# Optimization experiments

Measured on AMD Instinct MI355X. Metric: run time of the kernel, lower is better.

The kernel has to match this reference:

```python
import jax, jax.numpy as jnp
import numpy as np

B, S, DIM, H, DH = 1, 4096, 2048, 16, 128
EPS = 1e-5


def setup_inputs() -> dict:
    key = jax.random.key(0)
    ks = jax.random.split(key, 16)
    sc = 0.02
    inp = {
        'hidden_states': jax.random.normal(ks[0], (B, S, DIM), jnp.float32),
        'freqs_cos': jax.random.uniform(ks[1], (1, S, 1, DH), jnp.float32),
        'freqs_sin': jax.random.uniform(ks[2], (1, S, 1, DH), jnp.float32),
        'Wq': jax.random.normal(ks[3], (DIM, DIM), jnp.float32) * sc,
        'bq': jax.random.normal(ks[4], (DIM,), jnp.float32) * sc,
        'Wk': jax.random.normal(ks[5], (DIM, DIM), jnp.float32) * sc,
        'bk': jax.random.normal(ks[6], (DIM,), jnp.float32) * sc,
        'Wv': jax.random.normal(ks[7], (DIM, DIM), jnp.float32) * sc,
        'bv': jax.random.normal(ks[8], (DIM,), jnp.float32) * sc,
        'Wo': jax.random.normal(ks[9], (DIM, DIM), jnp.float32) * sc,
        'bo': jax.random.normal(ks[10], (DIM,), jnp.float32) * sc,
        'gq': jnp.ones((DIM,), jnp.float32),
        'gk': jnp.ones((DIM,), jnp.float32),
    }
    return inp


def _rmsnorm(x, g):
    var = jnp.mean(jnp.square(x), axis=-1, keepdims=True)
    return x * jax.lax.rsqrt(var + EPS) * g


def _apply_rope(x, freqs_cos, freqs_sin):
    # x: [B,S,H,DH]; interleaved rotary as in WanAttnProcessor
    x1 = x[..., 0::2]
    x2 = x[..., 1::2]
    cos = freqs_cos[..., 0::2]
    sin = freqs_sin[..., 1::2]
    o1 = x1 * cos - x2 * sin
    o2 = x1 * sin + x2 * cos
    return jnp.stack([o1, o2], axis=-1).reshape(x.shape)


def reference(hidden_states, freqs_cos, freqs_sin, Wq, bq, Wk, bk, Wv, bv, Wo, bo, gq, gk):
    q = hidden_states @ Wq + bq
    k = hidden_states @ Wk + bk
    v = hidden_states @ Wv + bv
    q = _rmsnorm(q, gq)
    k = _rmsnorm(k, gk)
    q = q.reshape(B, S, H, DH)
    k = k.reshape(B, S, H, DH)
    v = v.reshape(B, S, H, DH)
    q = _apply_rope(q, freqs_cos, freqs_sin)
    k = _apply_rope(k, freqs_cos, freqs_sin)
    scale = 1.0 / np.sqrt(DH).astype(np.float32)
    scores = jnp.einsum('bqhd,bkhd->bhqk', q, k) * scale
    attn = jax.nn.softmax(scores, axis=-1)
    out = jnp.einsum('bhqk,bkhd->bqhd', attn, v)
    out = out.reshape(B, S, H * DH)
    return out @ Wo + bo
```

## Files before the change

kernel.cpp:

```cpp
#include <hip/hip_runtime.h>
#include <hip/hip_bf16.h>

#define SEQ 4096
#define DIMC 2048
#define NH 16
#define DHD 128

typedef short s8v __attribute__((ext_vector_type(8)));
typedef float f4v __attribute__((ext_vector_type(4)));
typedef __bf16 bf8 __attribute__((ext_vector_type(8)));
typedef float f4 __attribute__((ext_vector_type(4)));

typedef __attribute__((address_space(3))) void lds_t;
typedef __attribute__((address_space(1))) void gbl_t;

__device__ __attribute__((aligned(256))) short g_h[(size_t)SEQ * DIMC];
__device__ __attribute__((aligned(256))) short g_q[(size_t)SEQ * DIMC];
__device__ __attribute__((aligned(256))) short g_k[(size_t)SEQ * DIMC];
__device__ __attribute__((aligned(256))) short g_v[(size_t)SEQ * DIMC];
__device__ __attribute__((aligned(256))) short g_vt[(size_t)DIMC * SEQ];
__device__ __attribute__((aligned(256))) short g_wt[4][(size_t)DIMC * DIMC];

__device__ __forceinline__ float b2f(short s) {
    union { unsigned u; float f; } v;
    v.u = ((unsigned)(unsigned short)s) << 16;
    return v.f;
}
__device__ __forceinline__ short f2b(float f) {
    union { float f; unsigned u; } v;
    v.f = f;
    unsigned b = v.u;
    b += 0x7FFFu + ((b >> 16) & 1u);
    return (short)(b >> 16);
}
__device__ __forceinline__ f4 mfma16(bf8 a, bf8 b, f4 c) {
    return __builtin_amdgcn_mfma_f32_16x16x32_bf16(a, b, c, 0, 0, 0);
}
__device__ __forceinline__ void gl_lds16(const short* g, short* l) {
    __builtin_amdgcn_global_load_lds((gbl_t*)g, (lds_t*)l, 16, 0, 0);
}

__global__ __launch_bounds__(256) void conv_h(const float* __restrict__ src) {
    size_t i = ((size_t)blockIdx.x * 256 + threadIdx.x) * 8;
    f4v u0 = *reinterpret_cast<const f4v*>(src + i);
    f4v u1 = *reinterpret_cast<const f4v*>(src + i + 4);
    s8v t;
    for (int j = 0; j < 4; ++j) { t[j] = f2b(u0[j]); t[4 + j] = f2b(u1[j]); }
    *reinterpret_cast<s8v*>(g_h + i) = t;
}

__global__ __launch_bounds__(256) void prep_w(const float* __restrict__ W0,
                                              const float* __restrict__ W1,
                                              const float* __restrict__ W2,
                                              const float* __restrict__ W3) {
    __shared__ __attribute__((aligned(16))) float t[64][68];
    const int z = blockIdx.z;
    const float* W = (z == 0) ? W0 : (z == 1) ? W1 : (z == 2) ? W2 : W3;
    short* WT = g_wt[z];
    const int r0 = blockIdx.y * 64, c0 = blockIdx.x * 64;
    const int tid = threadIdx.x;
    for (int i = 0; i < 4; ++i) {
        int slot = tid + i * 256;
        int r = slot >> 4, c4 = (slot & 15) * 4;
        *reinterpret_cast<f4v*>(&t[r][c4]) =
            *reinterpret_cast<const f4v*>(&W[(size_t)(r0 + r) * DIMC + c0 + c4]);
    }
    __syncthreads();
    for (int i = 0; i < 2; ++i) {
        int slot = tid + i * 256;
        int n = slot >> 3, k8 = (slot & 7) * 8;
        s8v o;
        for (int j = 0; j < 8; ++j) o[j] = f2b(t[k8 + j][n]);
        *reinterpret_cast<s8v*>(&WT[(size_t)(c0 + n) * DIMC + r0 + k8]) = o;
    }
}

template <int DSTF>
__device__ __forceinline__ void gemm_body(const short* __restrict__ X,
                                          const short* __restrict__ Bw,
                                          const float* __restrict__ bias,
                                          short* __restrict__ Yb,
                                          float* __restrict__ Yf,
                                          int bm, int bn) {
    __shared__ __attribute__((aligned(16))) short As[128 * 32];
    __shared__ __attribute__((aligned(16))) short Bs[128 * 32];
    const int tid = threadIdx.x;
    const int w = tid >> 6, lane = tid & 63;
    const int l16 = lane & 15, quad = lane >> 4;
    const int wm = w & 1, wn = w >> 1;

    f4 acc[4][4];
    for (int mi = 0; mi < 4; ++mi)
        for (int ni = 0; ni < 4; ++ni) acc[mi][ni] = (f4)0.0f;

    const int s0 = tid, s1 = tid + 256;
    const int ra0 = s0 >> 2, ca0 = (s0 & 3) * 8;
    const int ra1 = s1 >> 2, ca1 = (s1 & 3) * 8;
    const size_t xo0 = (size_t)(bm * 128 + ra0) * DIMC + ca0;
    const size_t xo1 = (size_t)(bm * 128 + ra1) * DIMC + ca1;
    const size_t bo0 = (size_t)(bn * 128 + ra0) * DIMC + ca0;
    const size_t bo1 = (size_t)(bn * 128 + ra1) * DIMC + ca1;
    short* lda0 = As + (size_t)(0 * 256 + w * 64) * 8;
    short* lda1 = As + (size_t)(1 * 256 + w * 64) * 8;
    short* ldb0 = Bs + (size_t)(0 * 256 + w * 64) * 8;
    short* ldb1 = Bs + (size_t)(1 * 256 + w * 64) * 8;

    for (int kb = 0; kb < DIMC; kb += 32) {
        __syncthreads();
        gl_lds16(X + xo0 + kb, lda0);
        gl_lds16(X + xo1 + kb, lda1);
        gl_lds16(Bw + bo0 + kb, ldb0);
        gl_lds16(Bw + bo1 + kb, ldb1);
        __syncthreads();
        bf8 af[4], bfr[4];
        for (int mi = 0; mi < 4; ++mi)
            af[mi] = *reinterpret_cast<const bf8*>(As + (wm * 64 + mi * 16 + l16) * 32 + quad * 8);
        for (int ni = 0; ni < 4; ++ni)
            bfr[ni] = *reinterpret_cast<const bf8*>(Bs + (wn * 64 + ni * 16 + l16) * 32 + quad * 8);
        for (int mi = 0; mi < 4; ++mi)
            for (int ni = 0; ni < 4; ++ni)
                acc[mi][ni] = mfma16(af[mi], bfr[ni], acc[mi][ni]);
    }

    for (int ni = 0; ni < 4; ++ni) {
        int col = bn * 128 + wn * 64 + ni * 16 + l16;
        float bcol = bias[col];
        for (int mi = 0; mi < 4; ++mi) {
            int row = bm * 128 + wm * 64 + mi * 16 + quad * 4;
            for (int r = 0; r < 4; ++r) {
                if (DSTF)
                    Yf[(size_t)(row + r) * DIMC + col] = acc[mi][ni][r] + bcol;
                else
                    Yb[(size_t)(row + r) * DIMC + col] = f2b(acc[mi][ni][r] + bcol);
            }
        }
    }
}

__global__ __launch_bounds__(256, 2) void gemm_qkv(const float* __restrict__ bq,
                                                   const float* __restrict__ bk,
                                                   const float* __restrict__ bv) {
    const int z = blockIdx.z;
    const float* bias = (z == 0) ? bq : (z == 1) ? bk : bv;
    short* Y = (z == 0) ? g_q : (z == 1) ? g_k : g_v;
    gemm_body<0>(g_h, g_wt[z], bias, Y, nullptr, blockIdx.y, blockIdx.x);
}

__global__ __launch_bounds__(256, 2) void gemm_o(const float* __restrict__ bias,
                                                 float* __restrict__ Yf) {
    gemm_body<1>(g_q, g_wt[3], bias, nullptr, Yf, blockIdx.y, blockIdx.x);
}

__global__ __launch_bounds__(256) void rmsnorm_rope(const float* __restrict__ gq,
                                                    const float* __restrict__ gk,
                                                    const float* __restrict__ fc,
                                                    const float* __restrict__ fs) {
    __shared__ float partial[4];
    __shared__ float totsh;
    const int s = blockIdx.x;
    const int which = blockIdx.y;
    short* x = which ? g_k : g_q;
    const float* g = which ? gk : gq;
    const int tid = threadIdx.x;
    const int d0 = tid * 8;

    s8v xv = *reinterpret_cast<const s8v*>(&x[(size_t)s * DIMC + d0]);
    float xf[8];
    float ssq = 0.0f;
    for (int j = 0; j < 8; ++j) { xf[j] = b2f(xv[j]); ssq += xf[j] * xf[j]; }
    for (int off = 32; off; off >>= 1) ssq += __shfl_down(ssq, off);
    if ((tid & 63) == 0) partial[tid >> 6] = ssq;
    __syncthreads();
    if (tid == 0) totsh = partial[0] + partial[1] + partial[2] + partial[3];
    __syncthreads();
    float rs = rsqrtf(totsh * (1.0f / (float)DIMC) + 1e-5f);
    if (which == 0) rs *= 0.12751744f;

    f4v g0 = *reinterpret_cast<const f4v*>(&g[d0]);
    f4v g1 = *reinterpret_cast<const f4v*>(&g[d0 + 4]);
    float xn[8];
    for (int j = 0; j < 4; ++j) { xn[j] = xf[j] * rs * g0[j]; xn[4 + j] = xf[4 + j] * rs * g1[j]; }

    s8v ov;
    for (int p = 0; p < 4; ++p) {
        int e = d0 + 2 * p;
        int hd = e & (DHD - 1);
        float c = fc[(size_t)s * DHD + hd];
        float sn = fs[(size_t)s * DHD + hd + 1];
        float x1 = xn[2 * p], x2 = xn[2 * p + 1];
        ov[2 * p]     = f2b(x1 * c - x2 * sn);
        ov[2 * p + 1] = f2b(x1 * sn + x2 * c);
    }
    *reinterpret_cast<s8v*>(&x[(size_t)s * DIMC + d0]) = ov;
}

__global__ __launch_bounds__(256) void transpose_v() {
    __shared__ __attribute__((aligned(16))) short t[64][72];
    const int h = blockIdx.z, dt = blockIdx.y, st = blockIdx.x;
    const int tid = threadIdx.x;
    const short* src = g_v + (size_t)st * 64 * DIMC + h * DHD + dt * 64;
    for (int i = 0; i < 2; ++i) {
        int slot = tid + i * 256;
        int s = slot >> 3, d8 = (slot & 7) * 8;
        *reinterpret_cast<s8v*>(&t[s][d8]) =
            *reinterpret_cast<const s8v*>(src + (size_t)s * DIMC + d8);
    }
    __syncthreads();
    short* dst = g_vt + (size_t)(h * DHD + dt * 64) * SEQ + st * 64;
    for (int i = 0; i < 2; ++i) {
        int slot = tid + i * 256;
        int d = slot >> 3, s8_ = (slot & 7) * 8;
        s8v o;
        for (int j = 0; j < 8; ++j) o[j] = t[s8_ + j][d];
        *reinterpret_cast<s8v*>(dst + (size_t)d * SEQ + s8_) = o;
    }
}

__global__ __launch_bounds__(256, 2) void attn_k() {
    __shared__ __attribute__((aligned(16))) short Ks0[2][64 * 128];
    __shared__ __attribute__((aligned(16))) short Vt0[2][128 * 64];
    __shared__ __attribute__((aligned(16))) __hip_bfloat16 Psb[4][16][72];

    const int h = blockIdx.y;
    const int q0 = blockIdx.x * 128;
    const int tid = threadIdx.x;
    const int w = tid >> 6, lane = tid & 63;
    const int l16 = lane & 15, quad = lane >> 4;

    bf8 qf[2][4];
    for (int qs = 0; qs < 2; ++qs) {
        const short* qb = g_q + (size_t)(q0 + w * 32 + qs * 16 + l16) * DIMC + h * DHD + quad * 8;
        for (int c = 0; c < 4; ++c)
            qf[qs][c] = *reinterpret_cast<const bf8*>(qb + c * 32);
    }
    f4 of[2][8];
    for (int qs = 0; qs < 2; ++qs)
        for (int n = 0; n < 8; ++n) of[qs][n] = (f4)0.0f;
    f4 lacc[2] = {(f4)0.0f, (f4)0.0f};

    s8v ob;
    for (int j = 0; j < 8; ++j) ob[j] = (short)0x3F80;
    const bf8 vones = __builtin_bit_cast(bf8, ob);

    const short* Kbase = g_k + h * DHD;
    const short* Vbase = g_vt + (size_t)h * DHD * SEQ;

    const short* kp[4];
    const short* vp[4];
    for (int i = 0; i < 4; ++i) {
        int s = tid + i * 256;
        int krow = s >> 4, kcb = ((s & 15) - krow) & 15;
        int vd = s >> 3, vkb = ((s & 7) - vd) & 7;
        kp[i] = Kbase + (size_t)krow * DIMC + kcb * 8;
        vp[i] = Vbase + (size_t)vd * SEQ + vkb * 8;
    }

    for (int i = 0; i < 4; ++i) {
        gl_lds16(kp[i], &Ks0[0][(size_t)(i * 256 + w * 64) * 8]);
        kp[i] += (size_t)64 * DIMC;
    }
    for (int i = 0; i < 4; ++i) {
        gl_lds16(vp[i], &Vt0[0][(size_t)(i * 256 + w * 64) * 8]);
        vp[i] += 64;
    }

    for (int kt = 0; kt < SEQ; kt += 64) {
        const int cur = (kt >> 6) & 1;
        if (kt + 64 < SEQ) {
            const int nxt = cur ^ 1;
            for (int i = 0; i < 4; ++i) {
                gl_lds16(kp[i], &Ks0[nxt][(size_t)(i * 256 + w * 64) * 8]);
                kp[i] += (size_t)64 * DIMC;
            }
            for (int i = 0; i < 4; ++i) {
                gl_lds16(vp[i], &Vt0[nxt][(size_t)(i * 256 + w * 64) * 8]);
                vp[i] += 64;
            }
            asm volatile("s_waitcnt vmcnt(8)" ::: "memory");
        } else {
            asm volatile("s_waitcnt vmcnt(0)" ::: "memory");
        }
        __builtin_amdgcn_sched_barrier(0);
        __builtin_amdgcn_s_barrier();
        __builtin_amdgcn_sched_barrier(0);

        const short* Ks = Ks0[cur];
        const short* Vt = Vt0[cur];

        f4 sa[2][4];
        for (int qs = 0; qs < 2; ++qs)
            for (int ns = 0; ns < 4; ++ns) sa[qs][ns] = (f4)0.0f;
        __builtin_amdgcn_s_setprio(1);
        for (int ns = 0; ns < 4; ++ns)
            for (int c = 0; c < 4; ++c) {
                bf8 kf = *reinterpret_cast<const bf8*>(
                    Ks + (ns * 16 + l16) * 128 + ((c * 4 + quad + l16) & 15) * 8);
                sa[0][ns] = mfma16(qf[0][c], kf, sa[0][ns]);
                sa[1][ns] = mfma16(qf[1][c], kf, sa[1][ns]);
            }
        __builtin_amdgcn_s_setprio(0);

        bf8 pa[2][2];
        for (int qs = 0; qs < 2; ++qs) {
            for (int ns = 0; ns < 4; ++ns) {
                float p0 = exp2f(sa[qs][ns][0]);
                float p1 = exp2f(sa[qs][ns][1]);
                float p2 = exp2f(sa[qs][ns][2]);
                float p3 = exp2f(sa[qs][ns][3]);
                __hip_bfloat162 c01 = __float22bfloat162_rn({p0, p1});
                __hip_bfloat162 c23 = __float22bfloat162_rn({p2, p3});
                int col = ns * 16 + l16;
                Psb[w][quad * 4 + 0][col] = c01.x;
                Psb[w][quad * 4 + 1][col] = c01.y;
                Psb[w][quad * 4 + 2][col] = c23.x;
                Psb[w][quad * 4 + 3][col] = c23.y;
            }
            asm volatile("s_waitcnt lgkmcnt(0)" ::: "memory");
            __builtin_amdgcn_sched_barrier(0);
            for (int c2 = 0; c2 < 2; ++c2)
                pa[qs][c2] = *reinterpret_cast<const bf8*>(&Psb[w][l16][c2 * 32 + quad * 8]);
        }

        __builtin_amdgcn_s_setprio(1);
        lacc[0] = mfma16(pa[0][0], vones, lacc[0]);
        lacc[0] = mfma16(pa[0][1], vones, lacc[0]);
        lacc[1] = mfma16(pa[1][0], vones, lacc[1]);
        lacc[1] = mfma16(pa[1][1], vones, lacc[1]);

        for (int c2 = 0; c2 < 2; ++c2)
            for (int n = 0; n < 8; ++n) {
                bf8 vf = *reinterpret_cast<const bf8*>(
                    Vt + (n * 16 + l16) * 64 + ((c2 * 4 + quad + l16) & 7) * 8);
                of[0][n] = mfma16(pa[0][c2], vf, of[0][n]);
                of[1][n] = mfma16(pa[1][c2], vf, of[1][n]);
            }
        __builtin_amdgcn_s_setprio(0);

        __builtin_amdgcn_s_barrier();
        __builtin_amdgcn_sched_barrier(0);
    }

    for (int qs = 0; qs < 2; ++qs)
        for (int r = 0; r < 4; ++r) {
            float inv = 1.0f / lacc[qs][r];
            int row = q0 + w * 32 + qs * 16 + quad * 4 + r;
            for (int n = 0; n < 8; ++n)
                g_q[(size_t)row * DIMC + h * DHD + n * 16 + l16] = f2b(of[qs][n][r] * inv);
        }
}

extern "C" void kernel_launch(void* const* d_in, const int* in_sizes, int n_in,
                              void* d_out, int out_size, void* d_ws, size_t ws_size,
                              hipStream_t stream) {
    const float* hidden = (const float*)d_in[0];
    const float* fc = (const float*)d_in[1];
    const float* fs = (const float*)d_in[2];
    const float* Wq = (const float*)d_in[3];
    const float* bq = (const float*)d_in[4];
    const float* Wk = (const float*)d_in[5];
    const float* bk = (const float*)d_in[6];
    const float* Wv = (const float*)d_in[7];
    const float* bv = (const float*)d_in[8];
    const float* Wo = (const float*)d_in[9];
    const float* bo = (const float*)d_in[10];
    const float* gq = (const float*)d_in[11];
    const float* gk = (const float*)d_in[12];

    dim3 blk(256);
    conv_h<<<dim3(4096), blk, 0, stream>>>(hidden);
    prep_w<<<dim3(32, 32, 4), blk, 0, stream>>>(Wq, Wk, Wv, Wo);
    gemm_qkv<<<dim3(16, 32, 3), blk, 0, stream>>>(bq, bk, bv);
    rmsnorm_rope<<<dim3(SEQ, 2), blk, 0, stream>>>(gq, gk, fc, fs);
    transpose_v<<<dim3(64, 2, NH), blk, 0, stream>>>();
    attn_k<<<dim3(32, NH), blk, 0, stream>>>();
    gemm_o<<<dim3(16, 32), blk, 0, stream>>>(bo, (float*)d_out);
}
```

Measured before the change: 540.2 us.

## Switch attention to 32x32x16 MFMA with register-only P transpose via permlane32 swap

```diff
diff --git a/kernel.cpp b/kernel.cpp
--- a/kernel.cpp
+++ b/kernel.cpp
@@ -10,6 +10,8 @@
 typedef float f4v __attribute__((ext_vector_type(4)));
 typedef __bf16 bf8 __attribute__((ext_vector_type(8)));
 typedef float f4 __attribute__((ext_vector_type(4)));
+typedef float f16v __attribute__((ext_vector_type(16)));
+typedef int i4v __attribute__((ext_vector_type(4)));
 
 typedef __attribute__((address_space(3))) void lds_t;
 typedef __attribute__((address_space(1))) void gbl_t;
@@ -36,8 +38,19 @@
 __device__ __forceinline__ f4 mfma16(bf8 a, bf8 b, f4 c) {
     return __builtin_amdgcn_mfma_f32_16x16x32_bf16(a, b, c, 0, 0, 0);
 }
+__device__ __forceinline__ f16v mfma32(bf8 a, bf8 b, f16v c) {
+    return __builtin_amdgcn_mfma_f32_32x32x16_bf16(a, b, c, 0, 0, 0);
+}
 __device__ __forceinline__ void gl_lds16(const short* g, short* l) {
     __builtin_amdgcn_global_load_lds((gbl_t*)g, (lds_t*)l, 16, 0, 0);
+}
+__device__ __forceinline__ void plane32_swap(int& a, int& b) {
+    asm volatile("v_permlane32_swap_b32 %0, %1" : "+v"(a), "+v"(b));
+}
+__device__ __forceinline__ int pk2b(float a, float b) {
+    int r;
+    asm("v_cvt_pk_bf16_f32 %0, %1, %2" : "=v"(r) : "v"(a), "v"(b));
+    return r;
 }
 
 __global__ __launch_bounds__(256) void conv_h(const float* __restrict__ src) {
@@ -219,26 +232,32 @@
 __global__ __launch_bounds__(256, 2) void attn_k() {
     __shared__ __attribute__((aligned(16))) short Ks0[2][64 * 128];
     __shared__ __attribute__((aligned(16))) short Vt0[2][128 * 64];
-    __shared__ __attribute__((aligned(16))) __hip_bfloat16 Psb[4][16][72];
 
     const int h = blockIdx.y;
     const int q0 = blockIdx.x * 128;
     const int tid = threadIdx.x;
     const int w = tid >> 6, lane = tid & 63;
-    const int l16 = lane & 15, quad = lane >> 4;
-
-    bf8 qf[2][4];
-    for (int qs = 0; qs < 2; ++qs) {
-        const short* qb = g_q + (size_t)(q0 + w * 32 + qs * 16 + l16) * DIMC + h * DHD + quad * 8;
-        for (int c = 0; c < 4; ++c)
-            qf[qs][c] = *reinterpret_cast<const bf8*>(qb + c * 32);
-    }
-    f4 of[2][8];
-    for (int qs = 0; qs < 2; ++qs)
-        for (int n = 0; n < 8; ++n) of[qs][n] = (f4)0.0f;
-    f4 lacc[2] = {(f4)0.0f, (f4)0.0f};
+    const int l32 = lane & 31, hf = lane >> 5;
+    const int l16 = lane & 15;
+    const int cbase = hf + l16;
+    const int khl = hf + l32;
+
+    bf8 qf[8];
+    {
+        const short* qb = g_q + (size_t)(q0 + w * 32 + l32) * DIMC + h * DHD + hf * 8;
+#pragma unroll
+        for (int dc = 0; dc < 8; ++dc)
+            qf[dc] = *reinterpret_cast<const bf8*>(qb + dc * 16);
+    }
+
+    f16v of[4];
+#pragma unroll
+    for (int i = 0; i < 4; ++i) of[i] = (f16v)0.0f;
+    f16v lacc = (f16v)0.0f;
+    const f16v fz = (f16v)0.0f;
 
     s8v ob;
+#pragma unroll
     for (int j = 0; j < 8; ++j) ob[j] = (short)0x3F80;
     const bf8 vones = __builtin_bit_cast(bf8, ob);
 
@@ -247,6 +266,7 @@
 
     const short* kp[4];
     const short* vp[4];
+#pragma unroll
     for (int i = 0; i < 4; ++i) {
         int s = tid + i * 256;
         int krow = s >> 4, kcb = ((s & 15) - krow) & 15;
@@ -255,10 +275,12 @@
         vp[i] = Vbase + (size_t)vd * SEQ + vkb * 8;
     }
 
+#pragma unroll
     for (int i = 0; i < 4; ++i) {
         gl_lds16(kp[i], &Ks0[0][(size_t)(i * 256 + w * 64) * 8]);
         kp[i] += (size_t)64 * DIMC;
     }
+#pragma unroll
     for (int i = 0; i < 4; ++i) {
         gl_lds16(vp[i], &Vt0[0][(size_t)(i * 256 + w * 64) * 8]);
         vp[i] += 64;
@@ -268,10 +290,12 @@
         const int cur = (kt >> 6) & 1;
         if (kt + 64 < SEQ) {
             const int nxt = cur ^ 1;
+#pragma unroll
             for (int i = 0; i < 4; ++i) {
                 gl_lds16(kp[i], &Ks0[nxt][(size_t)(i * 256 + w * 64) * 8]);
                 kp[i] += (size_t)64 * DIMC;
             }
+#pragma unroll
             for (int i = 0; i < 4; ++i) {
                 gl_lds16(vp[i], &Vt0[nxt][(size_t)(i * 256 + w * 64) * 8]);
                 vp[i] += 64;
@@ -287,66 +311,64 @@
         const short* Ks = Ks0[cur];
         const short* Vt = Vt0[cur];
 
-        f4 sa[2][4];
-        for (int qs = 0; qs < 2; ++qs)
-            for (int ns = 0; ns < 4; ++ns) sa[qs][ns] = (f4)0.0f;
-        __builtin_amdgcn_s_setprio(1);
-        for (int ns = 0; ns < 4; ++ns)
-            for (int c = 0; c < 4; ++c) {
-                bf8 kf = *reinterpret_cast<const bf8*>(
-                    Ks + (ns * 16 + l16) * 128 + ((c * 4 + quad + l16) & 15) * 8);
-                sa[0][ns] = mfma16(qf[0][c], kf, sa[0][ns]);
-                sa[1][ns] = mfma16(qf[1][c], kf, sa[1][ns]);
-            }
-        __builtin_amdgcn_s_setprio(0);
-
-        bf8 pa[2][2];
-        for (int qs = 0; qs < 2; ++qs) {
-            for (int ns = 0; ns < 4; ++ns) {
-                float p0 = exp2f(sa[qs][ns][0]);
-                float p1 = exp2f(sa[qs][ns][1]);
-                float p2 = exp2f(sa[qs][ns][2]);
-                float p3 = exp2f(sa[qs][ns][3]);
-                __hip_bfloat162 c01 = __float22bfloat162_rn({p0, p1});
-                __hip_bfloat162 c23 = __float22bfloat162_rn({p2, p3});
-                int col = ns * 16 + l16;
-                Psb[w][quad * 4 + 0][col] = c01.x;
-                Psb[w][quad * 4 + 1][col] = c01.y;
-                Psb[w][quad * 4 + 2][col] = c23.x;
-                Psb[w][quad * 4 + 3][col] = c23.y;
-            }
-            asm volatile("s_waitcnt lgkmcnt(0)" ::: "memory");
-            __builtin_amdgcn_sched_barrier(0);
-            for (int c2 = 0; c2 < 2; ++c2)
-                pa[qs][c2] = *reinterpret_cast<const bf8*>(&Psb[w][l16][c2 * 32 + quad * 8]);
+#pragma unroll
+        for (int kc = 0; kc < 2; ++kc) {
+            const short* krb = Ks + (kc * 32 + l32) * 128;
+            __builtin_amdgcn_s_setprio(1);
+            f16v sa = mfma32(*reinterpret_cast<const bf8*>(krb + ((cbase & 15) << 3)), qf[0], fz);
+#pragma unroll
+            for (int dc = 1; dc < 8; ++dc) {
+                bf8 kf = *reinterpret_cast<const bf8*>(krb + (((dc * 2 + cbase) & 15) << 3));
+                sa = mfma32(kf, qf[dc], sa);
+            }
+            __builtin_amdgcn_s_setprio(0);
+
+            int wv[8];
+#pragma unroll
+            for (int t = 0; t < 8; ++t) {
+                float e0 = exp2f(sa[2 * t]);
+                float e1 = exp2f(sa[2 * t + 1]);
+                wv[t] = pk2b(e0, e1);
+            }
+            int a0 = wv[0], b0 = wv[2]; plane32_swap(a0, b0);
+            int a1 = wv[1], b1 = wv[3]; plane32_swap(a1, b1);
+            int a2 = wv[4], b2 = wv[6]; plane32_swap(a2, b2);
+            int a3 = wv[5], b3 = wv[7]; plane32_swap(a3, b3);
+            i4v pw0 = {a0, a1, b0, b1};
+            i4v pw1 = {a2, a3, b2, b3};
+            bf8 pa0 = __builtin_bit_cast(bf8, pw0);
+            bf8 pa1 = __builtin_bit_cast(bf8, pw1);
+
+            __builtin_amdgcn_s_setprio(1);
+            lacc = mfma32(pa0, vones, lacc);
+            lacc = mfma32(pa1, vones, lacc);
+
+#pragma unroll
+            for (int kp2 = 0; kp2 < 2; ++kp2) {
+                bf8 pa = kp2 ? pa1 : pa0;
+#pragma unroll
+                for (int dcb = 0; dcb < 4; ++dcb) {
+                    int d = dcb * 32 + l32;
+                    int ks = (kc * 4 + kp2 * 2 + khl) & 7;
+                    bf8 vf = *reinterpret_cast<const bf8*>(Vt + d * 64 + ks * 8);
+                    of[dcb] = mfma32(pa, vf, of[dcb]);
+                }
+            }
+            __builtin_amdgcn_s_setprio(0);
         }
-
-        __builtin_amdgcn_s_setprio(1);
-        lacc[0] = mfma16(pa[0][0], vones, lacc[0]);
-        lacc[0] = mfma16(pa[0][1], vones, lacc[0]);
-        lacc[1] = mfma16(pa[1][0], vones, lacc[1]);
-        lacc[1] = mfma16(pa[1][1], vones, lacc[1]);
-
-        for (int c2 = 0; c2 < 2; ++c2)
-            for (int n = 0; n < 8; ++n) {
-                bf8 vf = *reinterpret_cast<const bf8*>(
-                    Vt + (n * 16 + l16) * 64 + ((c2 * 4 + quad + l16) & 7) * 8);
-                of[0][n] = mfma16(pa[0][c2], vf, of[0][n]);
-                of[1][n] = mfma16(pa[1][c2], vf, of[1][n]);
-            }
-        __builtin_amdgcn_s_setprio(0);
 
         __builtin_amdgcn_s_barrier();
         __builtin_amdgcn_sched_barrier(0);
     }
 
-    for (int qs = 0; qs < 2; ++qs)
-        for (int r = 0; r < 4; ++r) {
-            float inv = 1.0f / lacc[qs][r];
-            int row = q0 + w * 32 + qs * 16 + quad * 4 + r;
-            for (int n = 0; n < 8; ++n)
-                g_q[(size_t)row * DIMC + h * DHD + n * 16 + l16] = f2b(of[qs][n][r] * inv);
-        }
+#pragma unroll
+    for (int r = 0; r < 16; ++r) {
+        float iv = 1.0f / lacc[r];
+        int row = q0 + w * 32 + (r & 3) + 8 * (r >> 2) + 4 * hf;
+#pragma unroll
+        for (int dcb = 0; dcb < 4; ++dcb)
+            g_q[(size_t)row * DIMC + h * DHD + dcb * 32 + l32] = f2b(of[dcb][r] * iv);
+    }
 }
 
 extern "C" void kernel_launch(void* const* d_in, const int* in_sizes, int n_in,
```

Measured after the change: 538.6 us. Within noise of the previous version (-0.3%).
